# Kernel tuning notes

Measured on AMD Instinct MI355X. Metric: run time of the kernel, lower is better.

## Reference

```python
import jax, jax.numpy as jnp
import numpy as np

DIM = 768
HEADS = 12
HEAD_DIM = DIM // HEADS
HIDDEN = int(DIM * 4.0)
EPS = 1e-5


def layernorm(x, w, b):
    mu = jnp.mean(x, axis=-1, keepdims=True)
    var = jnp.var(x, axis=-1, keepdims=True)
    return (x - mu) * jax.lax.rsqrt(var + EPS) * w + b


def setup_inputs() -> dict:
    key = jax.random.key(0)
    ks = jax.random.split(key, 12)
    B, N = 4, 2048
    s = lambda fan_in: 1.0 / np.sqrt(fan_in)
    return {
        "x": jax.random.normal(ks[0], (B, N, DIM), dtype=jnp.float32),
        "qkv_w": jax.random.normal(ks[1], (3 * DIM, DIM), dtype=jnp.float32) * s(DIM),
        "proj_w": jax.random.normal(ks[2], (DIM, DIM), dtype=jnp.float32) * s(DIM),
        "proj_b": jnp.zeros((DIM,), dtype=jnp.float32),
        "norm1_w": jnp.ones((DIM,), dtype=jnp.float32),
        "norm1_b": jnp.zeros((DIM,), dtype=jnp.float32),
        "norm2_w": jnp.ones((DIM,), dtype=jnp.float32),
        "norm2_b": jnp.zeros((DIM,), dtype=jnp.float32),
        "fc1_w": jax.random.normal(ks[3], (HIDDEN, DIM), dtype=jnp.float32) * s(DIM),
        "fc1_b": jnp.zeros((HIDDEN,), dtype=jnp.float32),
        "fc2_w": jax.random.normal(ks[4], (DIM, HIDDEN), dtype=jnp.float32) * s(HIDDEN),
        "fc2_b": jnp.zeros((DIM,), dtype=jnp.float32),
    }


def reference(x, qkv_w, proj_w, proj_b, norm1_w, norm1_b, norm2_w, norm2_b,
              fc1_w, fc1_b, fc2_w, fc2_b):
    B, N, C = x.shape
    scale = HEAD_DIM ** -0.5
    shortcut = x
    h = layernorm(x, norm1_w, norm1_b)
    # qkv: [B, N, 3C] -> [3, B, H, N, Dh]
    qkv = (h @ qkv_w.T).reshape(B, N, 3, HEADS, HEAD_DIM)
    qkv = jnp.transpose(qkv, (2, 0, 3, 1, 4))
    q, k, v = qkv[0] * scale, qkv[1], qkv[2]
    attn = jnp.einsum("bhnd,bhmd->bhnm", q, k)
    attn = jax.nn.softmax(attn, axis=-1)
    out = jnp.einsum("bhnm,bhmd->bhnd", attn, v)
    out = jnp.transpose(out, (0, 2, 1, 3)).reshape(B, N, C)
    out = out @ proj_w.T + proj_b
    x = shortcut + out
    h2 = layernorm(x, norm2_w, norm2_b)
    mlp = jax.nn.gelu(h2 @ fc1_w.T + fc1_b, approximate=False) @ fc2_w.T + fc2_b
    return x + mlp
```

## Files before the change

### kernel.cpp

```cpp
#include <hip/hip_runtime.h>
#include <hip/hip_bf16.h>

#define SEQ   2048
#define NBAT  4
#define NH    12
#define HD    64
#define CDIM  768
#define HID   3072
#define NTOK  (SEQ*NBAT)

#define KS2 0.1803368801111244f

typedef __attribute__((ext_vector_type(8))) short short8;
typedef __attribute__((ext_vector_type(4))) float floatx4;

__device__ __forceinline__ float bf2f(unsigned short u) {
    union { unsigned int i; float f; } v; v.i = ((unsigned int)u) << 16; return v.f;
}
__device__ __forceinline__ unsigned short f2bf(float f) {
    union { float f; unsigned int i; } v; v.f = f;
    unsigned int i = v.i;
    return (unsigned short)((i + 0x7FFFu + ((i >> 16) & 1u)) >> 16);
}
__device__ __forceinline__ unsigned int fbits(float f) {
    union { float f; unsigned int i; } v; v.f = f; return v.i;
}
__device__ __forceinline__ float fast_exp2(float x) {
#if __has_builtin(__builtin_amdgcn_exp2f)
    return __builtin_amdgcn_exp2f(x);
#else
    return __expf(x * 0.69314718055994531f);
#endif
}
__device__ __forceinline__ float fast_rcp(float x) {
#if __has_builtin(__builtin_amdgcn_rcpf)
    return __builtin_amdgcn_rcpf(x);
#else
    return 1.f / x;
#endif
}
__device__ __forceinline__ float gelu_f(float v) {
    float u = 0.7978845608028654f * v * (1.f + 0.044715f * v * v);
    float e = fast_exp2(u * 2.885390081777927f);
    float th = 1.f - 2.f * fast_rcp(e + 1.f);
    return 0.5f * v * (1.f + th);
}
__device__ __forceinline__ void gload16(const unsigned short* g, unsigned short* l) {
    __builtin_amdgcn_global_load_lds(
        (const __attribute__((address_space(1))) unsigned int*)g,
        (__attribute__((address_space(3))) unsigned int*)l, 16, 0, 0);
}
__device__ __forceinline__ void pl32_swap(unsigned int& x, unsigned int& y) {
    asm("v_permlane32_swap_b32 %0, %1" : "+v"(x), "+v"(y));
}
__device__ __forceinline__ void pl16_swap(unsigned int& x, unsigned int& y) {
    asm("v_permlane16_swap_b32 %0, %1" : "+v"(x), "+v"(y));
}

__global__ __launch_bounds__(256) void cvt_all_kernel(
    const float* __restrict__ s0, const float* __restrict__ s1,
    const float* __restrict__ s2, const float* __restrict__ s3,
    unsigned short* __restrict__ d0, unsigned short* __restrict__ d1,
    unsigned short* __restrict__ d2, unsigned short* __restrict__ d3)
{
    int blk = blockIdx.x;
    const float* src; unsigned short* dst; int off;
    if (blk < 1728)      { src = s0; dst = d0; off = blk; }
    else if (blk < 2304) { src = s1; dst = d1; off = blk - 1728; }
    else if (blk < 4608) { src = s2; dst = d2; off = blk - 2304; }
    else                 { src = s3; dst = d3; off = blk - 4608; }
    int i = (off * 256 + threadIdx.x) * 4;
    float4 f = *(const float4*)(src + i);
    ushort4 o;
    o.x = f2bf(f.x); o.y = f2bf(f.y); o.z = f2bf(f.z); o.w = f2bf(f.w);
    *(ushort4*)(dst + i) = o;
}

__global__ __launch_bounds__(256) void ln_kernel(
    const float* __restrict__ x, const float* __restrict__ w,
    const float* __restrict__ b, unsigned short* __restrict__ y)
{
    int row  = blockIdx.x * 4 + (threadIdx.x >> 6);
    int lane = threadIdx.x & 63;
    const float4* xr = (const float4*)(x + (size_t)row * CDIM);
    float4 v[3];
    float s = 0.f, sq = 0.f;
#pragma unroll
    for (int i = 0; i < 3; i++) {
        float4 f = xr[lane + i * 64];
        v[i] = f;
        s  += (f.x + f.y) + (f.z + f.w);
        sq += (f.x * f.x + f.y * f.y) + (f.z * f.z + f.w * f.w);
    }
#pragma unroll
    for (int o = 32; o > 0; o >>= 1) {
        s  += __shfl_xor(s,  o, 64);
        sq += __shfl_xor(sq, o, 64);
    }
    float mean = s * (1.f / CDIM);
    float var  = sq * (1.f / CDIM) - mean * mean;
    float rstd = rsqrtf(var + 1e-5f);
    const float4* w4 = (const float4*)w;
    const float4* b4 = (const float4*)b;
    ushort4* y4 = (ushort4*)(y + (size_t)row * CDIM);
#pragma unroll
    for (int i = 0; i < 3; i++) {
        int c = lane + i * 64;
        float4 wf = w4[c], bf_ = b4[c];
        ushort4 o;
        o.x = f2bf((v[i].x - mean) * rstd * wf.x + bf_.x);
        o.y = f2bf((v[i].y - mean) * rstd * wf.y + bf_.y);
        o.z = f2bf((v[i].z - mean) * rstd * wf.z + bf_.z);
        o.w = f2bf((v[i].w - mean) * rstd * wf.w + bf_.w);
        y4[c] = o;
    }
}

#define BK 64

template<int ACT, int OUT32, int TM>
__global__ __launch_bounds__(256) void gemm_bt(
    const unsigned short* __restrict__ A, const unsigned short* __restrict__ W,
    const float* __restrict__ bias, const float* __restrict__ res,
    void* __restrict__ Cv, int M, int N, int K, int scol, float scale)
{
    constexpr int MT   = TM / 32;
    constexpr int ISSA = TM / 32;
    __shared__ __align__(16) unsigned short As[TM * BK];
    __shared__ __align__(16) unsigned short Bs[128 * BK];
    int tid  = threadIdx.x;
    int wave = tid >> 6, lane = tid & 63;
    int wr = wave >> 1, wc = wave & 1;
    int quad = lane >> 4, l15 = lane & 15;
    int m0 = blockIdx.x * TM, n0 = blockIdx.y * 128;

    int r8 = lane >> 3;
    int kc = (lane & 7) ^ r8;
    const unsigned short* Ag = A + (size_t)(m0 + wave * (TM / 4) + r8) * K + kc * 8;
    const unsigned short* Wg = W + (size_t)(n0 + wave * 32 + r8) * K + kc * 8;
    unsigned short* AsW = As + wave * (TM / 4) * BK;
    unsigned short* BsW = Bs + wave * 32 * BK;

    floatx4 acc[MT][4];
    floatx4 fz = {0.f, 0.f, 0.f, 0.f};
#pragma unroll
    for (int i = 0; i < MT; i++)
#pragma unroll
        for (int j = 0; j < 4; j++) acc[i][j] = fz;

    int sw = l15 & 7;
    for (int k0 = 0; k0 < K; k0 += BK) {
        __syncthreads();
#pragma unroll
        for (int j = 0; j < ISSA; j++)
            gload16(Ag + (size_t)(8 * j) * K + k0, AsW + j * 512);
#pragma unroll
        for (int j = 0; j < 4; j++)
            gload16(Wg + (size_t)(8 * j) * K + k0, BsW + j * 512);
        __syncthreads();

#pragma unroll
        for (int s = 0; s < 2; s++) {
            short8 af[MT], bfg[4];
            int ko = ((s * 4 + quad) ^ sw) * 8;
#pragma unroll
            for (int mt = 0; mt < MT; mt++)
                af[mt] = *(const short8*)(As + (wr * (TM / 2) + mt * 16 + l15) * BK + ko);
#pragma unroll
            for (int nt = 0; nt < 4; nt++)
                bfg[nt] = *(const short8*)(Bs + (wc * 64 + nt * 16 + l15) * BK + ko);
#pragma unroll
            for (int mt = 0; mt < MT; mt++)
#pragma unroll
                for (int nt = 0; nt < 4; nt++)
                    acc[mt][nt] = __builtin_amdgcn_mfma_f32_16x16x32_bf16(
                        af[mt], bfg[nt], acc[mt][nt], 0, 0, 0);
        }
    }

#pragma unroll
    for (int mt = 0; mt < MT; mt++) {
#pragma unroll
        for (int nt = 0; nt < 4; nt++) {
            int col = n0 + wc * 64 + nt * 16 + l15;
            float bv = bias ? bias[col] : 0.f;
            float cs = (col < scol) ? scale : 1.f;
#pragma unroll
            for (int r = 0; r < 4; r++) {
                int row = m0 + wr * (TM / 2) + mt * 16 + quad * 4 + r;
                size_t idx = (size_t)row * N + col;
                float v = acc[mt][nt][r] + bv;
                if (res) v += res[idx];
                if (ACT == 1) v = gelu_f(v);
                v *= cs;
                if (OUT32) ((float*)Cv)[idx] = v;
                else       ((unsigned short*)Cv)[idx] = f2bf(v);
            }
        }
    }
}

__global__ __launch_bounds__(256, 4) void attn_kernel(
    const unsigned short* __restrict__ qkv, unsigned short* __restrict__ out)
{
    __shared__ __align__(16) unsigned short Ks[2][64 * 64];
    __shared__ __align__(16) unsigned short Vt[2][64 * 72];

    int tid  = threadIdx.x;
    int wave = tid >> 6, lane = tid & 63;
    int quad = lane >> 4, l15 = lane & 15;
    int bh = blockIdx.y;
    int b  = bh / NH, h = bh % NH;
    size_t base = (size_t)b * SEQ * 2304 + h * 64;
    int qbase = blockIdx.x * 128 + wave * 32;

    short8 bq[2][2];
#pragma unroll
    for (int qh = 0; qh < 2; qh++)
#pragma unroll
        for (int kk = 0; kk < 2; kk++)
            bq[qh][kk] = *(const short8*)(qkv + base +
                (size_t)(qbase + qh * 16 + l15) * 2304 + kk * 32 + quad * 8);

    floatx4 o[2][4];
    floatx4 fz = {0.f, 0.f, 0.f, 0.f};
#pragma unroll
    for (int qh = 0; qh < 2; qh++)
#pragma unroll
        for (int dg = 0; dg < 4; dg++) o[qh][dg] = fz;
    float m2[2] = {-3e38f, -3e38f};
    float ls[2] = {0.f, 0.f};

    const unsigned short* kg = qkv + base + 768 +
        (size_t)(wave * 16 + (lane >> 3)) * 2304 + (((lane & 7) ^ ((lane >> 3) & 7)) * 8);
    const unsigned short* vptr = qkv + base + 1536;
    int vj  = tid & 31;
    int vd8 = wave * 16 + ((tid >> 5) & 1) * 8;
    int sw  = l15 & 7;

    gload16(kg, &Ks[0][wave * 1024]);
    gload16(kg + (size_t)8 * 2304, &Ks[0][wave * 1024 + 512]);
    {
        uint4 v0v = *(const uint4*)(vptr + (size_t)(2 * vj)     * 2304 + vd8);
        uint4 v1v = *(const uint4*)(vptr + (size_t)(2 * vj + 1) * 2304 + vd8);
        union { uint4 q; unsigned short u[8]; } u0, u1;
        u0.q = v0v; u1.q = v1v;
#pragma unroll
        for (int i = 0; i < 8; i++) {
            unsigned int w = (unsigned int)u0.u[i] | ((unsigned int)u1.u[i] << 16);
            *(unsigned int*)(&Vt[0][(vd8 + i) * 72 + 2 * vj]) = w;
        }
    }
    __syncthreads();

    for (int t = 0; t < SEQ / 64; t++) {
        int cur = t & 1, nxt = cur ^ 1;
        bool more = (t + 1 < SEQ / 64);
        uint4 v0v, v1v;
        if (more) {
            const unsigned short* kg2 = kg + (size_t)(t + 1) * 64 * 2304;
            gload16(kg2, &Ks[nxt][wave * 1024]);
            gload16(kg2 + (size_t)8 * 2304, &Ks[nxt][wave * 1024 + 512]);
            int kt = (t + 1) * 64;
            v0v = *(const uint4*)(vptr + (size_t)(kt + 2 * vj)     * 2304 + vd8);
            v1v = *(const uint4*)(vptr + (size_t)(kt + 2 * vj + 1) * 2304 + vd8);
        }

        floatx4 st[2][4];
        __builtin_amdgcn_s_setprio(1);
#pragma unroll
        for (int ts = 0; ts < 4; ts++) {
            short8 ak0 = *(const short8*)(&Ks[cur][(ts * 16 + l15) * 64 + (((0 * 4 + quad) ^ sw) * 8)]);
            short8 ak1 = *(const short8*)(&Ks[cur][(ts * 16 + l15) * 64 + (((1 * 4 + quad) ^ sw) * 8)]);
            floatx4 s0 = __builtin_amdgcn_mfma_f32_16x16x32_bf16(ak0, bq[0][0], fz, 0, 0, 0);
            s0 = __builtin_amdgcn_mfma_f32_16x16x32_bf16(ak1, bq[0][1], s0, 0, 0, 0);
            floatx4 s1 = __builtin_amdgcn_mfma_f32_16x16x32_bf16(ak0, bq[1][0], fz, 0, 0, 0);
            s1 = __builtin_amdgcn_mfma_f32_16x16x32_bf16(ak1, bq[1][1], s1, 0, 0, 0);
            st[0][ts] = s0; st[1][ts] = s1;
        }
        __builtin_amdgcn_s_setprio(0);

        unsigned int pw[2][4][2];
#pragma unroll
        for (int qh = 0; qh < 2; qh++) {
            float tm[4];
#pragma unroll
            for (int ts = 0; ts < 4; ts++)
                tm[ts] = fmaxf(fmaxf(st[qh][ts][0], st[qh][ts][1]),
                               fmaxf(st[qh][ts][2], st[qh][ts][3]));
            float tmax = fmaxf(fmaxf(tm[0], tm[1]), fmaxf(tm[2], tm[3]));
            tmax = fmaxf(tmax, __shfl_xor(tmax, 16, 64));
            tmax = fmaxf(tmax, __shfl_xor(tmax, 32, 64));
            if (!__all(tmax <= m2[qh] + 8.f)) {
                float nm = fmaxf(m2[qh], tmax);
                float alpha = fast_exp2(m2[qh] - nm);
                m2[qh] = nm;
                ls[qh] *= alpha;
#pragma unroll
                for (int dg = 0; dg < 4; dg++)
#pragma unroll
                    for (int r = 0; r < 4; r++) o[qh][dg][r] *= alpha;
            }
            float mm = m2[qh];
            float psum = 0.f;
#pragma unroll
            for (int ts = 0; ts < 4; ts++) {
                float p0 = fast_exp2(st[qh][ts][0] - mm);
                float p1 = fast_exp2(st[qh][ts][1] - mm);
                float p2 = fast_exp2(st[qh][ts][2] - mm);
                float p3 = fast_exp2(st[qh][ts][3] - mm);
                psum += (p0 + p1) + (p2 + p3);
                pw[qh][ts][0] = __builtin_amdgcn_perm(fbits(p1), fbits(p0), 0x07060302);
                pw[qh][ts][1] = __builtin_amdgcn_perm(fbits(p3), fbits(p2), 0x07060302);
            }
            ls[qh] += psum;
        }

#pragma unroll
        for (int hk = 0; hk < 2; hk++) {
            short8 bp[2];
#pragma unroll
            for (int qh = 0; qh < 2; qh++) {
                unsigned int x0 = pw[qh][2 * hk][0], y0 = pw[qh][2 * hk + 1][0];
                unsigned int x1 = pw[qh][2 * hk][1], y1 = pw[qh][2 * hk + 1][1];
                pl32_swap(x0, y0); pl16_swap(x0, y0);
                pl32_swap(x1, y1); pl16_swap(x1, y1);
                union { unsigned int u[4]; short8 s; } f;
                f.u[0] = x0; f.u[1] = x1; f.u[2] = y0; f.u[3] = y1;
                bp[qh] = f.s;
            }
            __builtin_amdgcn_s_setprio(1);
#pragma unroll
            for (int dg = 0; dg < 4; dg++) {
                short8 av = *(const short8*)(&Vt[cur][(dg * 16 + l15) * 72 + hk * 32 + quad * 8]);
                o[0][dg] = __builtin_amdgcn_mfma_f32_16x16x32_bf16(av, bp[0], o[0][dg], 0, 0, 0);
                o[1][dg] = __builtin_amdgcn_mfma_f32_16x16x32_bf16(av, bp[1], o[1][dg], 0, 0, 0);
            }
            __builtin_amdgcn_s_setprio(0);
        }

        if (more) {
            union { uint4 q; unsigned short u[8]; } u0, u1;
            u0.q = v0v; u1.q = v1v;
#pragma unroll
            for (int i = 0; i < 8; i++) {
                unsigned int w = (unsigned int)u0.u[i] | ((unsigned int)u1.u[i] << 16);
                *(unsigned int*)(&Vt[nxt][(vd8 + i) * 72 + 2 * vj]) = w;
            }
        }
        __syncthreads();
    }

#pragma unroll
    for (int qh = 0; qh < 2; qh++) {
        float l = ls[qh];
        l += __shfl_xor(l, 16, 64);
        l += __shfl_xor(l, 32, 64);
        float inv = 1.f / l;
        size_t orow = ((size_t)b * SEQ + qbase + qh * 16 + l15) * CDIM + h * 64;
#pragma unroll
        for (int dg = 0; dg < 4; dg++) {
            unsigned int u0 = (unsigned int)f2bf(o[qh][dg][0] * inv) | ((unsigned int)f2bf(o[qh][dg][1] * inv) << 16);
            unsigned int u1 = (unsigned int)f2bf(o[qh][dg][2] * inv) | ((unsigned int)f2bf(o[qh][dg][3] * inv) << 16);
            uint2 wv; wv.x = u0; wv.y = u1;
            *(uint2*)((unsigned short*)out + orow + dg * 16 + quad * 4) = wv;
        }
    }
}

extern "C" void kernel_launch(void* const* d_in, const int* in_sizes, int n_in,
                              void* d_out, int out_size, void* d_ws, size_t ws_size,
                              hipStream_t stream)
{
    const float* x      = (const float*)d_in[0];
    const float* qkv_w  = (const float*)d_in[1];
    const float* proj_w = (const float*)d_in[2];
    const float* proj_b = (const float*)d_in[3];
    const float* n1w    = (const float*)d_in[4];
    const float* n1b    = (const float*)d_in[5];
    const float* n2w    = (const float*)d_in[6];
    const float* n2b    = (const float*)d_in[7];
    const float* fc1w   = (const float*)d_in[8];
    const float* fc1b   = (const float*)d_in[9];
    const float* fc2w   = (const float*)d_in[10];
    const float* fc2b   = (const float*)d_in[11];
    float* out = (float*)d_out;

    unsigned short* ws = (unsigned short*)d_ws;
    unsigned short* wq = ws;
    unsigned short* wp = wq + 1769472;
    unsigned short* w1 = wp + 589824;
    unsigned short* w2 = w1 + 2359296;
    unsigned short* h    = w2 + 2359296;
    unsigned short* qkv  = h + 6291456;
    unsigned short* attn = qkv + 18874368;
    unsigned short* a    = qkv;

    dim3 blk(256);
    cvt_all_kernel<<<6912, blk, 0, stream>>>(qkv_w, proj_w, fc1w, fc2w, wq, wp, w1, w2);

    ln_kernel<<<NTOK / 4, blk, 0, stream>>>(x, n1w, n1b, h);
    gemm_bt<0, 0, 128><<<dim3(NTOK / 128, 2304 / 128), blk, 0, stream>>>(
        h, wq, nullptr, nullptr, qkv, NTOK, 2304, 768, 768, KS2);
    attn_kernel<<<dim3(SEQ / 128, NBAT * NH), blk, 0, stream>>>(qkv, attn);
    gemm_bt<0, 1, 64><<<dim3(NTOK / 64, 768 / 128), blk, 0, stream>>>(
        attn, wp, proj_b, x, out, NTOK, 768, 768, 0, 1.f);
    ln_kernel<<<NTOK / 4, blk, 0, stream>>>(out, n2w, n2b, h);
    gemm_bt<1, 0, 128><<<dim3(NTOK / 128, 3072 / 128), blk, 0, stream>>>(
        h, w1, fc1b, nullptr, a, NTOK, 3072, 768, 0, 1.f);
    gemm_bt<0, 1, 64><<<dim3(NTOK / 64, 768 / 128), blk, 0, stream>>>(
        a, w2, fc2b, out, out, NTOK, 768, 3072, 0, 1.f);
}
```

Baseline: 395.8 us.

## Replace GEMM with 256x256-tile, 8-wave, double-buffered pipelined MFMA kernel

Replaces the single-buffered 128-row GEMM with a 512-thread kernel that computes a 256x256 output tile per block. It double-buffers LDS across K-tiles, issues global loads for the next tile between MFMA phases, and uses explicit waitcnt, barriers and setprio to overlap memory with compute. Larger tiles raise data reuse per LDS load, but the projection GEMMs now launch only 32x3=96 blocks, which may underfill the GPU's CUs. Register pressure from 32 accumulator tiles per wave is also high.

```diff
diff --git a/kernel.cpp b/kernel.cpp
--- a/kernel.cpp
+++ b/kernel.cpp
@@ -116,80 +116,146 @@
     }
 }
 
-#define BK 64
-
-template<int ACT, int OUT32, int TM>
-__global__ __launch_bounds__(256) void gemm_bt(
+#define MFROW(I, AV)                                                              \
+    acc[I][0] = __builtin_amdgcn_mfma_f32_16x16x32_bf16(AV, b0, acc[I][0], 0,0,0);\
+    acc[I][1] = __builtin_amdgcn_mfma_f32_16x16x32_bf16(AV, b1, acc[I][1], 0,0,0);\
+    acc[I][2] = __builtin_amdgcn_mfma_f32_16x16x32_bf16(AV, b2, acc[I][2], 0,0,0);\
+    acc[I][3] = __builtin_amdgcn_mfma_f32_16x16x32_bf16(AV, b3, acc[I][3], 0,0,0);
+
+#define KTILE(CUR, KTv)                                                           \
+  {                                                                               \
+    const int ktn = (KTv) + 1; const bool more = (ktn < nk);                      \
+    short8 a0, a1, a2, a3, b0, b1, b2, b3;                                        \
+                 \
+    asm volatile("s_waitcnt vmcnt(4)" ::: "memory");                              \
+    __builtin_amdgcn_s_barrier();                                                 \
+    __builtin_amdgcn_sched_barrier(0);                                            \
+    if (more) {                                                                   \
+        gload16(agA0 + ktn * 64, &SA[(CUR)^1][0][ldst]);                          \
+        gload16(agA1 + ktn * 64, &SA[(CUR)^1][0][4096 + ldst]);                   \
+    }                                                                             \
+    b0 = *(const short8*)&SB[CUR][0][(rb     ) * 32 + slot];                      \
+    b1 = *(const short8*)&SB[CUR][0][(rb + 16) * 32 + slot];                      \
+    b2 = *(const short8*)&SB[CUR][0][(rb + 32) * 32 + slot];                      \
+    b3 = *(const short8*)&SB[CUR][0][(rb + 48) * 32 + slot];                      \
+    a0 = *(const short8*)&SA[CUR][0][(ra     ) * 32 + slot];                      \
+    a1 = *(const short8*)&SA[CUR][0][(ra + 16) * 32 + slot];                      \
+    a2 = *(const short8*)&SA[CUR][0][(ra + 32) * 32 + slot];                      \
+    a3 = *(const short8*)&SA[CUR][0][(ra + 48) * 32 + slot];                      \
+    asm volatile("s_waitcnt lgkmcnt(0)" ::: "memory");                            \
+    __builtin_amdgcn_sched_barrier(0);                                            \
+    __builtin_amdgcn_s_setprio(1);                                                \
+    MFROW(0, a0) MFROW(1, a1) MFROW(2, a2) MFROW(3, a3)                           \
+    __builtin_amdgcn_s_setprio(0);                                                \
+               \
+    if (more) {                                                                   \
+        gload16(wgB0 + ktn * 64, &SB[(CUR)^1][0][ldst]);                          \
+        gload16(wgB1 + ktn * 64, &SB[(CUR)^1][0][4096 + ldst]);                   \
+    }                                                                             \
+    a0 = *(const short8*)&SA[CUR][0][(ra +  64) * 32 + slot];                     \
+    a1 = *(const short8*)&SA[CUR][0][(ra +  80) * 32 + slot];                     \
+    a2 = *(const short8*)&SA[CUR][0][(ra +  96) * 32 + slot];                     \
+    a3 = *(const short8*)&SA[CUR][0][(ra + 112) * 32 + slot];                     \
+    asm volatile("s_waitcnt lgkmcnt(0)" ::: "memory");                            \
+    __builtin_amdgcn_sched_barrier(0);                                            \
+    __builtin_amdgcn_s_setprio(1);                                                \
+    MFROW(4, a0) MFROW(5, a1) MFROW(6, a2) MFROW(7, a3)                           \
+    __builtin_amdgcn_s_setprio(0);                                                \
+                 \
+    if (more) { asm volatile("s_waitcnt vmcnt(4)" ::: "memory"); }                \
+    else      { asm volatile("s_waitcnt vmcnt(0)" ::: "memory"); }                \
+    __builtin_amdgcn_s_barrier();                                                 \
+    __builtin_amdgcn_sched_barrier(0);                                            \
+    if (more) {                                                                   \
+        gload16(agA0 + ktn * 64 + 32, &SA[(CUR)^1][1][ldst]);                     \
+        gload16(agA1 + ktn * 64 + 32, &SA[(CUR)^1][1][4096 + ldst]);              \
+    }                                                                             \
+    b0 = *(const short8*)&SB[CUR][1][(rb     ) * 32 + slot];                      \
+    b1 = *(const short8*)&SB[CUR][1][(rb + 16) * 32 + slot];                      \
+    b2 = *(const short8*)&SB[CUR][1][(rb + 32) * 32 + slot];                      \
+    b3 = *(const short8*)&SB[CUR][1][(rb + 48) * 32 + slot];                      \
+    a0 = *(const short8*)&SA[CUR][1][(ra     ) * 32 + slot];                      \
+    a1 = *(const short8*)&SA[CUR][1][(ra + 16) * 32 + slot];                      \
+    a2 = *(const short8*)&SA[CUR][1][(ra + 32) * 32 + slot];                      \
+    a3 = *(const short8*)&SA[CUR][1][(ra + 48) * 32 + slot];                      \
+    asm volatile("s_waitcnt lgkmcnt(0)" ::: "memory");                            \
+    __builtin_amdgcn_sched_barrier(0);                                            \
+    __builtin_amdgcn_s_setprio(1);                                                \
+    MFROW(0, a0) MFROW(1, a1) MFROW(2, a2) MFROW(3, a3)                           \
+    __builtin_amdgcn_s_setprio(0);                                                \
+               \
+    if (more) {                                                                   \
+        gload16(wgB0 + ktn * 64 + 32, &SB[(CUR)^1][1][ldst]);                     \
+        gload16(wgB1 + ktn * 64 + 32, &SB[(CUR)^1][1][4096 + ldst]);              \
+    }                                                                             \
+    a0 = *(const short8*)&SA[CUR][1][(ra +  64) * 32 + slot];                     \
+    a1 = *(const short8*)&SA[CUR][1][(ra +  80) * 32 + slot];                     \
+    a2 = *(const short8*)&SA[CUR][1][(ra +  96) * 32 + slot];                     \
+    a3 = *(const short8*)&SA[CUR][1][(ra + 112) * 32 + slot];                     \
+    asm volatile("s_waitcnt lgkmcnt(0)" ::: "memory");                            \
+    __builtin_amdgcn_sched_barrier(0);                                            \
+    __builtin_amdgcn_s_setprio(1);                                                \
+    MFROW(4, a0) MFROW(5, a1) MFROW(6, a2) MFROW(7, a3)                           \
+    __builtin_amdgcn_s_setprio(0);                                                \
+  }
+
+template<int ACT, int OUT32>
+__global__ __launch_bounds__(512, 2) void gemm8(
     const unsigned short* __restrict__ A, const unsigned short* __restrict__ W,
     const float* __restrict__ bias, const float* __restrict__ res,
     void* __restrict__ Cv, int M, int N, int K, int scol, float scale)
 {
-    constexpr int MT   = TM / 32;
-    constexpr int ISSA = TM / 32;
-    __shared__ __align__(16) unsigned short As[TM * BK];
-    __shared__ __align__(16) unsigned short Bs[128 * BK];
+    __shared__ __align__(16) unsigned short SA[2][2][8192];
+    __shared__ __align__(16) unsigned short SB[2][2][8192];
+
     int tid  = threadIdx.x;
     int wave = tid >> 6, lane = tid & 63;
-    int wr = wave >> 1, wc = wave & 1;
+    int wm = wave >> 2, wn = wave & 3;
     int quad = lane >> 4, l15 = lane & 15;
-    int m0 = blockIdx.x * TM, n0 = blockIdx.y * 128;
-
-    int r8 = lane >> 3;
-    int kc = (lane & 7) ^ r8;
-    const unsigned short* Ag = A + (size_t)(m0 + wave * (TM / 4) + r8) * K + kc * 8;
-    const unsigned short* Wg = W + (size_t)(n0 + wave * 32 + r8) * K + kc * 8;
-    unsigned short* AsW = As + wave * (TM / 4) * BK;
-    unsigned short* BsW = Bs + wave * 32 * BK;
-
-    floatx4 acc[MT][4];
+    int m0 = blockIdx.x * 256, n0 = blockIdx.y * 256;
+
+    int sr = tid >> 2;
+    int sc = (tid & 3) ^ (sr & 3);
+    const unsigned short* agA0 = A + (size_t)(m0 +   0 + sr) * K + sc * 8;
+    const unsigned short* agA1 = A + (size_t)(m0 + 128 + sr) * K + sc * 8;
+    const unsigned short* wgB0 = W + (size_t)(n0 +   0 + sr) * K + sc * 8;
+    const unsigned short* wgB1 = W + (size_t)(n0 + 128 + sr) * K + sc * 8;
+    unsigned int ldst = wave * 512;
+
+    floatx4 acc[8][4];
     floatx4 fz = {0.f, 0.f, 0.f, 0.f};
 #pragma unroll
-    for (int i = 0; i < MT; i++)
+    for (int i = 0; i < 8; i++)
 #pragma unroll
         for (int j = 0; j < 4; j++) acc[i][j] = fz;
 
-    int sw = l15 & 7;
-    for (int k0 = 0; k0 < K; k0 += BK) {
-        __syncthreads();
-#pragma unroll
-        for (int j = 0; j < ISSA; j++)
-            gload16(Ag + (size_t)(8 * j) * K + k0, AsW + j * 512);
-#pragma unroll
-        for (int j = 0; j < 4; j++)
-            gload16(Wg + (size_t)(8 * j) * K + k0, BsW + j * 512);
-        __syncthreads();
-
-#pragma unroll
-        for (int s = 0; s < 2; s++) {
-            short8 af[MT], bfg[4];
-            int ko = ((s * 4 + quad) ^ sw) * 8;
-#pragma unroll
-            for (int mt = 0; mt < MT; mt++)
-                af[mt] = *(const short8*)(As + (wr * (TM / 2) + mt * 16 + l15) * BK + ko);
-#pragma unroll
-            for (int nt = 0; nt < 4; nt++)
-                bfg[nt] = *(const short8*)(Bs + (wc * 64 + nt * 16 + l15) * BK + ko);
-#pragma unroll
-            for (int mt = 0; mt < MT; mt++)
-#pragma unroll
-                for (int nt = 0; nt < 4; nt++)
-                    acc[mt][nt] = __builtin_amdgcn_mfma_f32_16x16x32_bf16(
-                        af[mt], bfg[nt], acc[mt][nt], 0, 0, 0);
-        }
-    }
-
-#pragma unroll
-    for (int mt = 0; mt < MT; mt++) {
-#pragma unroll
-        for (int nt = 0; nt < 4; nt++) {
-            int col = n0 + wc * 64 + nt * 16 + l15;
+    int slot = (quad ^ (l15 & 3)) * 8;
+    int ra = wm * 128 + l15;
+    int rb = wn * 64  + l15;
+    int nk = K >> 6;
+
+    gload16(agA0, &SA[0][0][ldst]);        gload16(agA1, &SA[0][0][4096 + ldst]);
+    gload16(wgB0, &SB[0][0][ldst]);        gload16(wgB1, &SB[0][0][4096 + ldst]);
+    gload16(agA0 + 32, &SA[0][1][ldst]);   gload16(agA1 + 32, &SA[0][1][4096 + ldst]);
+    gload16(wgB0 + 32, &SB[0][1][ldst]);   gload16(wgB1 + 32, &SB[0][1][4096 + ldst]);
+
+    for (int kt = 0; kt < nk; kt += 2) {
+        KTILE(0, kt)
+        KTILE(1, kt + 1)
+    }
+
+#pragma unroll
+    for (int i = 0; i < 8; i++) {
+#pragma unroll
+        for (int j = 0; j < 4; j++) {
+            int col = n0 + wn * 64 + j * 16 + l15;
             float bv = bias ? bias[col] : 0.f;
             float cs = (col < scol) ? scale : 1.f;
 #pragma unroll
             for (int r = 0; r < 4; r++) {
-                int row = m0 + wr * (TM / 2) + mt * 16 + quad * 4 + r;
+                int row = m0 + wm * 128 + i * 16 + quad * 4 + r;
                 size_t idx = (size_t)row * N + col;
-                float v = acc[mt][nt][r] + bv;
+                float v = acc[i][j][r] + bv;
                 if (res) v += res[idx];
                 if (ACT == 1) v = gelu_f(v);
                 v *= cs;
@@ -397,17 +463,18 @@
     unsigned short* a    = qkv;
 
     dim3 blk(256);
+    dim3 blk8(512);
     cvt_all_kernel<<<6912, blk, 0, stream>>>(qkv_w, proj_w, fc1w, fc2w, wq, wp, w1, w2);
 
     ln_kernel<<<NTOK / 4, blk, 0, stream>>>(x, n1w, n1b, h);
-    gemm_bt<0, 0, 128><<<dim3(NTOK / 128, 2304 / 128), blk, 0, stream>>>(
+    gemm8<0, 0><<<dim3(NTOK / 256, 2304 / 256), blk8, 0, stream>>>(
         h, wq, nullptr, nullptr, qkv, NTOK, 2304, 768, 768, KS2);
     attn_kernel<<<dim3(SEQ / 128, NBAT * NH), blk, 0, stream>>>(qkv, attn);
-    gemm_bt<0, 1, 64><<<dim3(NTOK / 64, 768 / 128), blk, 0, stream>>>(
+    gemm8<0, 1><<<dim3(NTOK / 256, 768 / 256), blk8, 0, stream>>>(
         attn, wp, proj_b, x, out, NTOK, 768, 768, 0, 1.f);
     ln_kernel<<<NTOK / 4, blk, 0, stream>>>(out, n2w, n2b, h);
-    gemm_bt<1, 0, 128><<<dim3(NTOK / 128, 3072 / 128), blk, 0, stream>>>(
+    gemm8<1, 0><<<dim3(NTOK / 256, 3072 / 256), blk8, 0, stream>>>(
         h, w1, fc1b, nullptr, a, NTOK, 3072, 768, 0, 1.f);
-    gemm_bt<0, 1, 64><<<dim3(NTOK / 64, 768 / 128), blk, 0, stream>>>(
+    gemm8<0, 1><<<dim3(NTOK / 256, 768 / 256), blk8, 0, stream>>>(
         a, w2, fc2b, out, out, NTOK, 768, 3072, 0, 1.f);
 }
```

Result: slower. 530.7 us (+34.1%).
